# Kernel tuning notes

Hardware: AMD Instinct MI355X
Metric: run time of the kernel (lower is better)

Reference implementation:

```python
import jax, jax.numpy as jnp
import numpy as np

B, D, H = 1024, 64, 512


def setup_inputs() -> dict:
    key = jax.random.key(0)
    ks = jax.random.split(key, 6)
    sc = lambda fan_in: 1.0 / np.sqrt(fan_in)
    return {
        "x_t": jax.random.normal(ks[0], (B, D), jnp.float32),
        "t": jax.random.uniform(ks[1], (B, 1), dtype=jnp.float32),
        "beta": jax.random.uniform(ks[2], (B, 1), dtype=jnp.float32),
        "W1": jax.random.normal(ks[3], (D + 1, H), jnp.float32) * sc(D + 1),
        "b1": jnp.zeros((H,), jnp.float32),
        "W2": jax.random.normal(ks[4], (H, H), jnp.float32) * sc(H),
        "b2": jnp.zeros((H,), jnp.float32),
        "W3": jax.random.normal(ks[5], (H, D), jnp.float32) * sc(H),
        "b3": jnp.zeros((D,), jnp.float32),
    }


def _score(W1, b1, W2, b2, W3, b3, x, t):
    # x: [D], t: [1] -> s: [D]; small tanh MLP score network s(x, t)
    h = jnp.tanh(jnp.concatenate([x, t]) @ W1 + b1)
    h = jnp.tanh(h @ W2 + b2)
    return h @ W3 + b3


def reference(x_t, t, beta, W1, b1, W2, b2, W3, b3):
    def per_sample(x, tt):
        s_x = lambda xx: _score(W1, b1, W2, b2, W3, b3, xx, tt)
        s_t_fn = lambda ttt: _score(W1, b1, W2, b2, W3, b3, x, ttt)

        # s_t = grad(sum(s), t): sum over output dims of ds/dt (forward-mode JVP)
        _, s_dot = jax.jvp(s_t_fn, (tt,), (jnp.ones_like(tt),))
        s_t = jnp.sum(s_dot)  # scalar per sample

        # phi(x) = div_x s + |s|^2 + <s, x>; loss term = grad_x phi (2nd order through div)
        def phi(xx):
            jac = jax.jacfwd(s_x)(xx)          # [D, D]
            div = jnp.trace(jac)
            s = s_x(xx)
            return div + jnp.sum(s * s) + jnp.dot(s, xx)

        g = jax.grad(phi)(x)  # [D]
        return s_t, g

    s_t, g = jax.vmap(per_sample)(x_t, t)  # s_t: [B], g: [B, D]
    # loss = mean_D |s_t - 0.5 * beta * grad|, shape [B, 1]
    return jnp.mean(jnp.abs(s_t[:, None] - 0.5 * beta * g), axis=1, keepdims=True)
```

## Files before the change

### kernel.cpp

```cpp
#include <hip/hip_runtime.h>
#include <math.h>


#define Bsz 1024
#define Dd  64
#define Hh  512

__global__ __launch_bounds__(256) void kpre(const float* __restrict__ W1,
                                            const float* __restrict__ W3,
                                            const float* __restrict__ W2,
                                            float* __restrict__ C,
                                            float* __restrict__ W3T,
                                            float* __restrict__ W1xT,
                                            float* __restrict__ w3sum,
                                            float* __restrict__ s_t) {
  const int b = blockIdx.x;
  const int tid = threadIdx.x;
  if (b < 64) {
    __shared__ float W1s[64][68];
    __shared__ float W3s[64][68];
    const int bj = (b & 7) * 64, bl = (b >> 3) * 64;
    for (int q = 0; q < 16; q++) {
      int idx = tid + q * 256;
      int i = idx >> 6, j = idx & 63;
      W1s[i][j] = W1[i * Hh + bj + j];
    }
    for (int q = 0; q < 16; q++) {
      int idx = tid + q * 256;
      int l = idx >> 6, i = idx & 63;
      W3s[i][l] = W3[(bl + l) * Dd + i];
    }
    __syncthreads();
    const int tj = (tid >> 4) << 2, tl = (tid & 15) << 2;
    float acc[4][4] = {};
#pragma unroll 8
    for (int i = 0; i < 64; i++) {
      float4 a = *(const float4*)&W1s[i][tj];
      float4 bb = *(const float4*)&W3s[i][tl];
      float ar[4] = {a.x, a.y, a.z, a.w};
      float br[4] = {bb.x, bb.y, bb.z, bb.w};
#pragma unroll
      for (int r = 0; r < 4; r++)
#pragma unroll
        for (int c = 0; c < 4; c++) acc[r][c] += ar[r] * br[c];
    }
#pragma unroll
    for (int r = 0; r < 4; r++) {
      int j = bj + tj + r;
      float4 cv;
#pragma unroll
      for (int c = 0; c < 4; c++)
        ((float*)&cv)[c] = W2[j * Hh + bl + tl + c] * acc[r][c];
      *(float4*)&C[j * Hh + bl + tl] = cv;
    }
  } else {
    int gid = (b - 64) * 256 + tid;
#pragma unroll
    for (int q = 0; q < 8; q++) {
      int e = gid + q * 4096;
      int l = e >> 6, k = e & 63;
      W3T[k * Hh + l] = W3[e];
    }
#pragma unroll
    for (int q = 0; q < 8; q++) {
      int e = gid + q * 4096;
      int i = e >> 9, j = e & 511;
      W1xT[j * Dd + i] = W1[e];
    }
    if (gid < Hh) {
      float sacc = 0.f;
      for (int k = 0; k < 64; k++) sacc += W3[gid * Dd + k];
      w3sum[gid] = sacc;
    }
    if (gid < Bsz) s_t[gid] = 0.f;
  }
}

__global__ __launch_bounds__(256) void k1_h1(const float* __restrict__ X,
                                             const float* __restrict__ tt,
                                             const float* __restrict__ W1,
                                             const float* __restrict__ b1,
                                             float* __restrict__ h1,
                                             float* __restrict__ a1,
                                             float* __restrict__ dh1t) {
  __shared__ float As[64][68];
  __shared__ float Bs[64][68];
  const int i0 = blockIdx.x * 64, n0 = blockIdx.y * 64;
  const int tid = threadIdx.x;
  for (int q = 0; q < 16; q++) {
    int idx = tid + q * 256;
    int i = idx >> 6, k = idx & 63;
    As[k][i] = X[(i0 + i) * Dd + k];
  }
  for (int q = 0; q < 16; q++) {
    int idx = tid + q * 256;
    int k = idx >> 6, n = idx & 63;
    Bs[k][n] = W1[k * Hh + n0 + n];
  }
  __syncthreads();
  const int ti = (tid >> 4) << 2, tn = (tid & 15) << 2;
  float acc[4][4] = {};
#pragma unroll 8
  for (int k = 0; k < 64; k++) {
    float4 a = *(const float4*)&As[k][ti];
    float4 b = *(const float4*)&Bs[k][tn];
    float ar[4] = {a.x, a.y, a.z, a.w};
    float br[4] = {b.x, b.y, b.z, b.w};
#pragma unroll
    for (int r = 0; r < 4; r++)
#pragma unroll
      for (int c = 0; c < 4; c++) acc[r][c] += ar[r] * br[c];
  }
  const int nb = n0 + tn;
  float4 wtv = *(const float4*)&W1[Dd * Hh + nb];
  float4 b1v = *(const float4*)&b1[nb];
#pragma unroll
  for (int r = 0; r < 4; r++) {
    int i = i0 + ti + r;
    float tv = tt[i];
    float4 hv, av, dv;
#pragma unroll
    for (int c = 0; c < 4; c++) {
      float wt = ((float*)&wtv)[c];
      float z = acc[r][c] + tv * wt + ((float*)&b1v)[c];
      float h = tanhf(z);
      float a = 1.f - h * h;
      ((float*)&hv)[c] = h;
      ((float*)&av)[c] = a;
      ((float*)&dv)[c] = a * wt;
    }
    *(float4*)&h1[i * Hh + nb] = hv;
    *(float4*)&a1[i * Hh + nb] = av;
    *(float4*)&dh1t[i * Hh + nb] = dv;
  }
}

__global__ __launch_bounds__(256) void k2_h2(const float* __restrict__ h1,
                                             const float* __restrict__ dh1t,
                                             const float* __restrict__ W2,
                                             const float* __restrict__ b2,
                                             const float* __restrict__ w3s,
                                             float* __restrict__ h2,
                                             float* __restrict__ a2,
                                             float* __restrict__ s_t) {
  __shared__ float A1s[32][36], A2s[32][36], Bs[32][68];
  const int i0 = blockIdx.x * 32, n0 = blockIdx.y * 64;
  const int tid = threadIdx.x;
  const int ti = (tid >> 4) << 1, tn = (tid & 15) << 2;
  const int ai = tid >> 5, ak = tid & 31;
  const int bk = tid >> 6, bn = tid & 63;
  float ra1[4], ra2[4], rb[8];
#pragma unroll
  for (int q = 0; q < 4; q++) {
    ra1[q] = h1[(i0 + ai + q * 8) * Hh + ak];
    ra2[q] = dh1t[(i0 + ai + q * 8) * Hh + ak];
  }
#pragma unroll
  for (int q = 0; q < 8; q++) rb[q] = W2[(bk + q * 4) * Hh + n0 + bn];
  float acc1[2][4] = {}, acc2[2][4] = {};
  for (int c = 0; c < 16; c++) {
    __syncthreads();
#pragma unroll
    for (int q = 0; q < 4; q++) {
      A1s[ak][ai + q * 8] = ra1[q];
      A2s[ak][ai + q * 8] = ra2[q];
    }
#pragma unroll
    for (int q = 0; q < 8; q++) Bs[bk + q * 4][bn] = rb[q];
    __syncthreads();
    if (c < 15) {
      int k0 = (c + 1) * 32;
#pragma unroll
      for (int q = 0; q < 4; q++) {
        ra1[q] = h1[(i0 + ai + q * 8) * Hh + k0 + ak];
        ra2[q] = dh1t[(i0 + ai + q * 8) * Hh + k0 + ak];
      }
#pragma unroll
      for (int q = 0; q < 8; q++) rb[q] = W2[(k0 + bk + q * 4) * Hh + n0 + bn];
    }
#pragma unroll 8
    for (int k = 0; k < 32; k++) {
      float2 a1v = *(const float2*)&A1s[k][ti];
      float2 a2v = *(const float2*)&A2s[k][ti];
      float4 bv = *(const float4*)&Bs[k][tn];
      float ar1[2] = {a1v.x, a1v.y}, ar2[2] = {a2v.x, a2v.y};
      float br[4] = {bv.x, bv.y, bv.z, bv.w};
#pragma unroll
      for (int r = 0; r < 2; r++)
#pragma unroll
        for (int cc = 0; cc < 4; cc++) {
          acc1[r][cc] += ar1[r] * br[cc];
          acc2[r][cc] += ar2[r] * br[cc];
        }
    }
  }
  const int nb = n0 + tn;
  float4 b2v = *(const float4*)&b2[nb];
  float4 w3v = *(const float4*)&w3s[nb];
#pragma unroll
  for (int r = 0; r < 2; r++) {
    int i = i0 + ti + r;
    float4 hv, av;
    float part = 0.f;
#pragma unroll
    for (int cc = 0; cc < 4; cc++) {
      float z = acc1[r][cc] + ((float*)&b2v)[cc];
      float h = tanhf(z);
      float a = 1.f - h * h;
      ((float*)&hv)[cc] = h;
      ((float*)&av)[cc] = a;
      part += a * acc2[r][cc] * ((float*)&w3v)[cc];
    }
    *(float4*)&h2[i * Hh + nb] = hv;
    *(float4*)&a2[i * Hh + nb] = av;
#pragma unroll
    for (int off = 1; off < 16; off <<= 1) part += __shfl_xor(part, off, 64);
    if ((tid & 15) == 0) atomicAdd(&s_t[i], part);
  }
}

__global__ __launch_bounds__(256) void k34_s_r3(const float* __restrict__ h2,
                                                const float* __restrict__ W3,
                                                const float* __restrict__ W3T,
                                                const float* __restrict__ b3,
                                                const float* __restrict__ X,
                                                float* __restrict__ s,
                                                float* __restrict__ r3) {
  int i = (blockIdx.x * 256 + threadIdx.x) >> 6;
  int lam = threadIdx.x & 63;
  float sacc = b3[lam];
#pragma unroll
  for (int c = 0; c < 8; c++) {
    float hv = h2[i * Hh + c * 64 + lam];
#pragma unroll 8
    for (int k = 0; k < 64; k++) {
      float h = __shfl(hv, k, 64);
      sacc += h * W3[(c * 64 + k) * Dd + lam];
    }
  }
  s[i * Dd + lam] = sacc;
  float yv = 2.f * sacc + X[i * Dd + lam];
#pragma unroll
  for (int c = 0; c < 8; c++) {
    float acc = 0.f;
#pragma unroll 8
    for (int k = 0; k < 64; k++) {
      float yk = __shfl(yv, k, 64);
      acc += yk * W3T[k * Hh + c * 64 + lam];
    }
    r3[i * Hh + c * 64 + lam] = acc;
  }
}

__global__ __launch_bounds__(256) void k4b_ut2(const float* __restrict__ a1,
                                               const float* __restrict__ a2,
                                               const float* __restrict__ h2,
                                               const float* __restrict__ r3,
                                               const float* __restrict__ C,
                                               float* __restrict__ u,
                                               float* __restrict__ t2) {
  __shared__ float A1s[32][36], A2s[32][36], Bus[32][68], Bvs[32][68];
  const int i0 = blockIdx.x * 32, n0 = blockIdx.y * 64;
  const int tid = threadIdx.x;
  const int ti = (tid >> 4) << 1, tn = (tid & 15) << 2;
  const int ai = tid >> 5, ak = tid & 31;
  const int bk = tid >> 6, bn = tid & 63;
  const int un = tid >> 5, uk = tid & 31;
  float ra1[4], ra2[4], rbu[8], rbv[8];
#pragma unroll
  for (int q = 0; q < 4; q++) {
    ra2[q] = a2[(i0 + ai + q * 8) * Hh + ak];
    ra1[q] = a1[(i0 + ai + q * 8) * Hh + ak];
  }
#pragma unroll
  for (int q = 0; q < 8; q++) {
    rbu[q] = C[(n0 + un + q * 8) * Hh + uk];
    rbv[q] = C[(bk + q * 4) * Hh + n0 + bn];
  }
  float accU[2][4] = {}, accV[2][4] = {};
  for (int c = 0; c < 16; c++) {
    __syncthreads();
#pragma unroll
    for (int q = 0; q < 4; q++) {
      A1s[ak][ai + q * 8] = ra1[q];
      A2s[ak][ai + q * 8] = ra2[q];
    }
#pragma unroll
    for (int q = 0; q < 8; q++) {
      Bus[uk][un + q * 8] = rbu[q];
      Bvs[bk + q * 4][bn] = rbv[q];
    }
    __syncthreads();
    if (c < 15) {
      int k0 = (c + 1) * 32;
#pragma unroll
      for (int q = 0; q < 4; q++) {
        ra2[q] = a2[(i0 + ai + q * 8) * Hh + k0 + ak];
        ra1[q] = a1[(i0 + ai + q * 8) * Hh + k0 + ak];
      }
#pragma unroll
      for (int q = 0; q < 8; q++) {
        rbu[q] = C[(n0 + un + q * 8) * Hh + k0 + uk];
        rbv[q] = C[(k0 + bk + q * 4) * Hh + n0 + bn];
      }
    }
#pragma unroll 8
    for (int k = 0; k < 32; k++) {
      float2 a2v = *(const float2*)&A2s[k][ti];
      float2 a1v = *(const float2*)&A1s[k][ti];
      float4 bu = *(const float4*)&Bus[k][tn];
      float4 bv = *(const float4*)&Bvs[k][tn];
      float ar2[2] = {a2v.x, a2v.y}, ar1[2] = {a1v.x, a1v.y};
      float bur[4] = {bu.x, bu.y, bu.z, bu.w};
      float bvr[4] = {bv.x, bv.y, bv.z, bv.w};
#pragma unroll
      for (int r = 0; r < 2; r++)
#pragma unroll
        for (int cc = 0; cc < 4; cc++) {
          accU[r][cc] += ar2[r] * bur[cc];
          accV[r][cc] += ar1[r] * bvr[cc];
        }
    }
  }
  const int nb = n0 + tn;
#pragma unroll
  for (int r = 0; r < 2; r++) {
    int i = i0 + ti + r;
    float4 a2f = *(const float4*)&a2[i * Hh + nb];
    float4 h2f = *(const float4*)&h2[i * Hh + nb];
    float4 r3f = *(const float4*)&r3[i * Hh + nb];
    float4 uv, t2v;
#pragma unroll
    for (int cc = 0; cc < 4; cc++) {
      ((float*)&uv)[cc] = accU[r][cc];
      ((float*)&t2v)[cc] = ((float*)&a2f)[cc] *
          (((float*)&r3f)[cc] - 2.f * ((float*)&h2f)[cc] * accV[r][cc]);
    }
    *(float4*)&u[i * Hh + nb] = uv;
    *(float4*)&t2[i * Hh + nb] = t2v;
  }
}

__global__ __launch_bounds__(256) void k5_p(const float* __restrict__ t2,
                                            const float* __restrict__ W2,
                                            const float* __restrict__ a1,
                                            const float* __restrict__ h1,
                                            const float* __restrict__ u,
                                            float* __restrict__ p) {
  __shared__ float As[32][36], Bts[32][68];
  const int i0 = blockIdx.x * 32, n0 = blockIdx.y * 64;
  const int tid = threadIdx.x;
  const int ti = (tid >> 4) << 1, tn = (tid & 15) << 2;
  const int ai = tid >> 5, ak = tid & 31;
  const int un = tid >> 5, uk = tid & 31;
  float ra[4], rb[8];
#pragma unroll
  for (int q = 0; q < 4; q++) ra[q] = t2[(i0 + ai + q * 8) * Hh + ak];
#pragma unroll
  for (int q = 0; q < 8; q++) rb[q] = W2[(n0 + un + q * 8) * Hh + uk];
  float acc[2][4] = {};
  for (int c = 0; c < 16; c++) {
    __syncthreads();
#pragma unroll
    for (int q = 0; q < 4; q++) As[ak][ai + q * 8] = ra[q];
#pragma unroll
    for (int q = 0; q < 8; q++) Bts[uk][un + q * 8] = rb[q];
    __syncthreads();
    if (c < 15) {
      int k0 = (c + 1) * 32;
#pragma unroll
      for (int q = 0; q < 4; q++) ra[q] = t2[(i0 + ai + q * 8) * Hh + k0 + ak];
#pragma unroll
      for (int q = 0; q < 8; q++) rb[q] = W2[(n0 + un + q * 8) * Hh + k0 + uk];
    }
#pragma unroll 8
    for (int k = 0; k < 32; k++) {
      float2 av = *(const float2*)&As[k][ti];
      float4 bv = *(const float4*)&Bts[k][tn];
      float ar[2] = {av.x, av.y};
      float br[4] = {bv.x, bv.y, bv.z, bv.w};
#pragma unroll
      for (int r = 0; r < 2; r++)
#pragma unroll
        for (int cc = 0; cc < 4; cc++) acc[r][cc] += ar[r] * br[cc];
    }
  }
  const int nb = n0 + tn;
#pragma unroll
  for (int r = 0; r < 2; r++) {
    int i = i0 + ti + r;
    float4 a1f = *(const float4*)&a1[i * Hh + nb];
    float4 h1f = *(const float4*)&h1[i * Hh + nb];
    float4 uf  = *(const float4*)&u[i * Hh + nb];
    float4 pv;
#pragma unroll
    for (int cc = 0; cc < 4; cc++)
      ((float*)&pv)[cc] = ((float*)&a1f)[cc] *
          (acc[r][cc] - 2.f * ((float*)&h1f)[cc] * ((float*)&uf)[cc]);
    *(float4*)&p[i * Hh + nb] = pv;
  }
}

__global__ __launch_bounds__(256) void k6_loss(const float* __restrict__ p,
                                               const float* __restrict__ W1xT,
                                               const float* __restrict__ s,
                                               const float* __restrict__ s_t,
                                               const float* __restrict__ beta,
                                               float* __restrict__ out) {
  int i = (blockIdx.x * 256 + threadIdx.x) >> 6;
  int lam = threadIdx.x & 63;
  float g = s[i * Dd + lam];
#pragma unroll
  for (int c = 0; c < 8; c++) {
    float pv = p[i * Hh + c * 64 + lam];
#pragma unroll 8
    for (int jj = 0; jj < 64; jj++) {
      float pj = __shfl(pv, jj, 64);
      g += pj * W1xT[(c * 64 + jj) * Dd + lam];
    }
  }
  float e = fabsf(s_t[i] - 0.5f * beta[i] * g);
#pragma unroll
  for (int off = 32; off; off >>= 1) e += __shfl_down(e, off, 64);
  if (lam == 0) out[i] = e * (1.f / 64.f);
}

extern "C" void kernel_launch(void* const* d_in, const int* in_sizes, int n_in,
                              void* d_out, int out_size, void* d_ws, size_t ws_size,
                              hipStream_t stream) {
  const float* X    = (const float*)d_in[0];
  const float* tt   = (const float*)d_in[1];
  const float* beta = (const float*)d_in[2];
  const float* W1   = (const float*)d_in[3];
  const float* b1   = (const float*)d_in[4];
  const float* W2   = (const float*)d_in[5];
  const float* b2   = (const float*)d_in[6];
  const float* W3   = (const float*)d_in[7];
  const float* b3   = (const float*)d_in[8];
  float* out = (float*)d_out;

  float* ws   = (float*)d_ws;
  float* C    = ws;
  float* W3T  = C + 262144;
  float* W1xT = W3T + 32768;
  float* w3s  = W1xT + 32768;
  float* h1   = w3s + 512;
  float* a1   = h1 + 524288;
  float* dh1t = a1 + 524288;
  float* h2   = dh1t + 524288;
  float* a2v  = h2 + 524288;
  float* r3   = a2v + 524288;
  float* uu   = r3 + 524288;
  float* t2   = uu + 524288;
  float* pp   = t2 + 524288;
  float* ss   = pp + 524288;
  float* st   = ss + 65536;

  kpre<<<80, 256, 0, stream>>>(W1, W3, W2, C, W3T, W1xT, w3s, st);
  k1_h1<<<dim3(16, 8), 256, 0, stream>>>(X, tt, W1, b1, h1, a1, dh1t);
  k2_h2<<<dim3(32, 8), 256, 0, stream>>>(h1, dh1t, W2, b2, w3s, h2, a2v, st);
  k34_s_r3<<<256, 256, 0, stream>>>(h2, W3, W3T, b3, X, ss, r3);
  k4b_ut2<<<dim3(32, 8), 256, 0, stream>>>(a1, a2v, h2, r3, C, uu, t2);
  k5_p<<<dim3(32, 8), 256, 0, stream>>>(t2, W2, a1, h1, uu, pp);
  k6_loss<<<256, 256, 0, stream>>>(pp, W1xT, ss, st, beta, out);
}
```

Baseline: 239.8 us.

## Fuse per-sample forward/backward pipeline into one kernel with shared-memory activations

Replaces six launches (h1, h2, s/r3, u/t2, p, loss) with a single kernel in which each 512-thread block handles 4 samples and keeps all intermediate activations in shared memory. The goal is to drop the global-memory round trips for the many [B,H] intermediates, the launch overheads, and the atomics used for s_t. In exchange, every block streams the full W1, W2, W3 and C weight matrices from global or L2 for only 4 samples, so weight reuse per block is much lower and the work becomes matrix-vector-like. Some C reads are column-strided (C[k*Hh+n0]) while others are row reads that are not coalesced across threads.

```diff
diff --git a/kernel.cpp b/kernel.cpp
--- a/kernel.cpp
+++ b/kernel.cpp
@@ -10,10 +10,7 @@
                                             const float* __restrict__ W3,
                                             const float* __restrict__ W2,
                                             float* __restrict__ C,
-                                            float* __restrict__ W3T,
-                                            float* __restrict__ W1xT,
-                                            float* __restrict__ w3sum,
-                                            float* __restrict__ s_t) {
+                                            float* __restrict__ w3sum) {
   const int b = blockIdx.x;
   const int tid = threadIdx.x;
   if (b < 64) {
@@ -54,375 +51,223 @@
       *(float4*)&C[j * Hh + bl + tl] = cv;
     }
   } else {
-    int gid = (b - 64) * 256 + tid;
-#pragma unroll
-    for (int q = 0; q < 8; q++) {
-      int e = gid + q * 4096;
-      int l = e >> 6, k = e & 63;
-      W3T[k * Hh + l] = W3[e];
-    }
-#pragma unroll
-    for (int q = 0; q < 8; q++) {
-      int e = gid + q * 4096;
-      int i = e >> 9, j = e & 511;
-      W1xT[j * Dd + i] = W1[e];
-    }
-    if (gid < Hh) {
+#pragma unroll
+    for (int r = 0; r < 2; r++) {
+      int n = tid + r * 256;
       float sacc = 0.f;
-      for (int k = 0; k < 64; k++) sacc += W3[gid * Dd + k];
-      w3sum[gid] = sacc;
-    }
-    if (gid < Bsz) s_t[gid] = 0.f;
+#pragma unroll 4
+      for (int k4 = 0; k4 < 16; k4++) {
+        float4 w = *(const float4*)&W3[n * Dd + k4 * 4];
+        sacc += w.x; sacc += w.y; sacc += w.z; sacc += w.w;
+      }
+      w3sum[n] = sacc;
+    }
   }
 }
 
-__global__ __launch_bounds__(256) void k1_h1(const float* __restrict__ X,
-                                             const float* __restrict__ tt,
-                                             const float* __restrict__ W1,
-                                             const float* __restrict__ b1,
-                                             float* __restrict__ h1,
-                                             float* __restrict__ a1,
-                                             float* __restrict__ dh1t) {
-  __shared__ float As[64][68];
-  __shared__ float Bs[64][68];
-  const int i0 = blockIdx.x * 64, n0 = blockIdx.y * 64;
+__global__ __launch_bounds__(512) void kfused(const float* __restrict__ X,
+                                              const float* __restrict__ tt,
+                                              const float* __restrict__ beta,
+                                              const float* __restrict__ W1,
+                                              const float* __restrict__ b1,
+                                              const float* __restrict__ W2,
+                                              const float* __restrict__ b2,
+                                              const float* __restrict__ W3,
+                                              const float* __restrict__ b3,
+                                              const float* __restrict__ C,
+                                              const float* __restrict__ w3sum,
+                                              float* __restrict__ out) {
+  __shared__ float xs[Dd * 4], ys[Dd * 4];
+  __shared__ float h1s[Hh * 4], a1s[Hh * 4], q1s[Hh * 4];
+  __shared__ float h2s[Hh * 4], a2s[Hh * 4], t2s[Hh * 4], ps[Hh * 4];
+  __shared__ float sts[4], tb[4], bb4[4], red[32];
+  __shared__ float ph[512];
+
   const int tid = threadIdx.x;
-  for (int q = 0; q < 16; q++) {
-    int idx = tid + q * 256;
-    int i = idx >> 6, k = idx & 63;
-    As[k][i] = X[(i0 + i) * Dd + k];
-  }
-  for (int q = 0; q < 16; q++) {
-    int idx = tid + q * 256;
-    int k = idx >> 6, n = idx & 63;
-    Bs[k][n] = W1[k * Hh + n0 + n];
-  }
-  __syncthreads();
-  const int ti = (tid >> 4) << 2, tn = (tid & 15) << 2;
-  float acc[4][4] = {};
-#pragma unroll 8
-  for (int k = 0; k < 64; k++) {
-    float4 a = *(const float4*)&As[k][ti];
-    float4 b = *(const float4*)&Bs[k][tn];
-    float ar[4] = {a.x, a.y, a.z, a.w};
-    float br[4] = {b.x, b.y, b.z, b.w};
-#pragma unroll
-    for (int r = 0; r < 4; r++)
-#pragma unroll
-      for (int c = 0; c < 4; c++) acc[r][c] += ar[r] * br[c];
-  }
-  const int nb = n0 + tn;
-  float4 wtv = *(const float4*)&W1[Dd * Hh + nb];
-  float4 b1v = *(const float4*)&b1[nb];
-#pragma unroll
-  for (int r = 0; r < 4; r++) {
-    int i = i0 + ti + r;
-    float tv = tt[i];
-    float4 hv, av, dv;
-#pragma unroll
-    for (int c = 0; c < 4; c++) {
-      float wt = ((float*)&wtv)[c];
-      float z = acc[r][c] + tv * wt + ((float*)&b1v)[c];
+  const int s0 = blockIdx.x * 4;
+  const int n0 = tid;
+  const int dd = tid & 63;
+  const int half = (tid >> 6) & 1;
+  const int ss = tid >> 7;
+
+  if (tid < 256) {
+    int sA = tid >> 6, dA = tid & 63;
+    xs[dA * 4 + sA] = X[(s0 + sA) * Dd + dA];
+  }
+  if (tid < 4) tb[tid] = tt[s0 + tid];
+  else if (tid < 8) bb4[tid - 4] = beta[s0 + tid - 4];
+  __syncthreads();
+
+  {
+    float acc[4] = {};
+#pragma unroll 8
+    for (int k = 0; k < Dd; k++) {
+      float w = W1[k * Hh + n0];
+      float4 xv = *(const float4*)&xs[k * 4];
+#pragma unroll
+      for (int s = 0; s < 4; s++) acc[s] += w * ((float*)&xv)[s];
+    }
+    float wt = W1[Dd * Hh + n0];
+    float bc = b1[n0];
+    float4 hv, av, qv;
+#pragma unroll
+    for (int s = 0; s < 4; s++) {
+      float z = acc[s] + tb[s] * wt + bc;
       float h = tanhf(z);
       float a = 1.f - h * h;
-      ((float*)&hv)[c] = h;
-      ((float*)&av)[c] = a;
-      ((float*)&dv)[c] = a * wt;
-    }
-    *(float4*)&h1[i * Hh + nb] = hv;
-    *(float4*)&a1[i * Hh + nb] = av;
-    *(float4*)&dh1t[i * Hh + nb] = dv;
-  }
-}
-
-__global__ __launch_bounds__(256) void k2_h2(const float* __restrict__ h1,
-                                             const float* __restrict__ dh1t,
-                                             const float* __restrict__ W2,
-                                             const float* __restrict__ b2,
-                                             const float* __restrict__ w3s,
-                                             float* __restrict__ h2,
-                                             float* __restrict__ a2,
-                                             float* __restrict__ s_t) {
-  __shared__ float A1s[32][36], A2s[32][36], Bs[32][68];
-  const int i0 = blockIdx.x * 32, n0 = blockIdx.y * 64;
-  const int tid = threadIdx.x;
-  const int ti = (tid >> 4) << 1, tn = (tid & 15) << 2;
-  const int ai = tid >> 5, ak = tid & 31;
-  const int bk = tid >> 6, bn = tid & 63;
-  float ra1[4], ra2[4], rb[8];
-#pragma unroll
-  for (int q = 0; q < 4; q++) {
-    ra1[q] = h1[(i0 + ai + q * 8) * Hh + ak];
-    ra2[q] = dh1t[(i0 + ai + q * 8) * Hh + ak];
-  }
-#pragma unroll
-  for (int q = 0; q < 8; q++) rb[q] = W2[(bk + q * 4) * Hh + n0 + bn];
-  float acc1[2][4] = {}, acc2[2][4] = {};
-  for (int c = 0; c < 16; c++) {
-    __syncthreads();
-#pragma unroll
-    for (int q = 0; q < 4; q++) {
-      A1s[ak][ai + q * 8] = ra1[q];
-      A2s[ak][ai + q * 8] = ra2[q];
-    }
-#pragma unroll
-    for (int q = 0; q < 8; q++) Bs[bk + q * 4][bn] = rb[q];
-    __syncthreads();
-    if (c < 15) {
-      int k0 = (c + 1) * 32;
-#pragma unroll
-      for (int q = 0; q < 4; q++) {
-        ra1[q] = h1[(i0 + ai + q * 8) * Hh + k0 + ak];
-        ra2[q] = dh1t[(i0 + ai + q * 8) * Hh + k0 + ak];
-      }
-#pragma unroll
-      for (int q = 0; q < 8; q++) rb[q] = W2[(k0 + bk + q * 4) * Hh + n0 + bn];
-    }
-#pragma unroll 8
-    for (int k = 0; k < 32; k++) {
-      float2 a1v = *(const float2*)&A1s[k][ti];
-      float2 a2v = *(const float2*)&A2s[k][ti];
-      float4 bv = *(const float4*)&Bs[k][tn];
-      float ar1[2] = {a1v.x, a1v.y}, ar2[2] = {a2v.x, a2v.y};
-      float br[4] = {bv.x, bv.y, bv.z, bv.w};
-#pragma unroll
-      for (int r = 0; r < 2; r++)
-#pragma unroll
-        for (int cc = 0; cc < 4; cc++) {
-          acc1[r][cc] += ar1[r] * br[cc];
-          acc2[r][cc] += ar2[r] * br[cc];
-        }
-    }
-  }
-  const int nb = n0 + tn;
-  float4 b2v = *(const float4*)&b2[nb];
-  float4 w3v = *(const float4*)&w3s[nb];
-#pragma unroll
-  for (int r = 0; r < 2; r++) {
-    int i = i0 + ti + r;
+      ((float*)&hv)[s] = h;
+      ((float*)&av)[s] = a;
+      ((float*)&qv)[s] = a * wt;
+    }
+    *(float4*)&h1s[n0 * 4] = hv;
+    *(float4*)&a1s[n0 * 4] = av;
+    *(float4*)&q1s[n0 * 4] = qv;
+  }
+  __syncthreads();
+
+  {
+    float acc1[4] = {}, acc2[4] = {};
+#pragma unroll 8
+    for (int k = 0; k < Hh; k++) {
+      float w = W2[k * Hh + n0];
+      float4 hv = *(const float4*)&h1s[k * 4];
+      float4 qv = *(const float4*)&q1s[k * 4];
+#pragma unroll
+      for (int s = 0; s < 4; s++) {
+        acc1[s] += w * ((float*)&hv)[s];
+        acc2[s] += w * ((float*)&qv)[s];
+      }
+    }
+    float bc = b2[n0], wc = w3sum[n0];
+    float stp[4];
     float4 hv, av;
-    float part = 0.f;
-#pragma unroll
-    for (int cc = 0; cc < 4; cc++) {
-      float z = acc1[r][cc] + ((float*)&b2v)[cc];
+#pragma unroll
+    for (int s = 0; s < 4; s++) {
+      float z = acc1[s] + bc;
       float h = tanhf(z);
       float a = 1.f - h * h;
-      ((float*)&hv)[cc] = h;
-      ((float*)&av)[cc] = a;
-      part += a * acc2[r][cc] * ((float*)&w3v)[cc];
-    }
-    *(float4*)&h2[i * Hh + nb] = hv;
-    *(float4*)&a2[i * Hh + nb] = av;
-#pragma unroll
-    for (int off = 1; off < 16; off <<= 1) part += __shfl_xor(part, off, 64);
-    if ((tid & 15) == 0) atomicAdd(&s_t[i], part);
-  }
-}
-
-__global__ __launch_bounds__(256) void k34_s_r3(const float* __restrict__ h2,
-                                                const float* __restrict__ W3,
-                                                const float* __restrict__ W3T,
-                                                const float* __restrict__ b3,
-                                                const float* __restrict__ X,
-                                                float* __restrict__ s,
-                                                float* __restrict__ r3) {
-  int i = (blockIdx.x * 256 + threadIdx.x) >> 6;
-  int lam = threadIdx.x & 63;
-  float sacc = b3[lam];
-#pragma unroll
-  for (int c = 0; c < 8; c++) {
-    float hv = h2[i * Hh + c * 64 + lam];
-#pragma unroll 8
-    for (int k = 0; k < 64; k++) {
-      float h = __shfl(hv, k, 64);
-      sacc += h * W3[(c * 64 + k) * Dd + lam];
-    }
-  }
-  s[i * Dd + lam] = sacc;
-  float yv = 2.f * sacc + X[i * Dd + lam];
-#pragma unroll
-  for (int c = 0; c < 8; c++) {
-    float acc = 0.f;
-#pragma unroll 8
-    for (int k = 0; k < 64; k++) {
-      float yk = __shfl(yv, k, 64);
-      acc += yk * W3T[k * Hh + c * 64 + lam];
-    }
-    r3[i * Hh + c * 64 + lam] = acc;
-  }
-}
-
-__global__ __launch_bounds__(256) void k4b_ut2(const float* __restrict__ a1,
-                                               const float* __restrict__ a2,
-                                               const float* __restrict__ h2,
-                                               const float* __restrict__ r3,
-                                               const float* __restrict__ C,
-                                               float* __restrict__ u,
-                                               float* __restrict__ t2) {
-  __shared__ float A1s[32][36], A2s[32][36], Bus[32][68], Bvs[32][68];
-  const int i0 = blockIdx.x * 32, n0 = blockIdx.y * 64;
-  const int tid = threadIdx.x;
-  const int ti = (tid >> 4) << 1, tn = (tid & 15) << 2;
-  const int ai = tid >> 5, ak = tid & 31;
-  const int bk = tid >> 6, bn = tid & 63;
-  const int un = tid >> 5, uk = tid & 31;
-  float ra1[4], ra2[4], rbu[8], rbv[8];
-#pragma unroll
-  for (int q = 0; q < 4; q++) {
-    ra2[q] = a2[(i0 + ai + q * 8) * Hh + ak];
-    ra1[q] = a1[(i0 + ai + q * 8) * Hh + ak];
-  }
-#pragma unroll
-  for (int q = 0; q < 8; q++) {
-    rbu[q] = C[(n0 + un + q * 8) * Hh + uk];
-    rbv[q] = C[(bk + q * 4) * Hh + n0 + bn];
-  }
-  float accU[2][4] = {}, accV[2][4] = {};
-  for (int c = 0; c < 16; c++) {
-    __syncthreads();
-#pragma unroll
-    for (int q = 0; q < 4; q++) {
-      A1s[ak][ai + q * 8] = ra1[q];
-      A2s[ak][ai + q * 8] = ra2[q];
-    }
-#pragma unroll
-    for (int q = 0; q < 8; q++) {
-      Bus[uk][un + q * 8] = rbu[q];
-      Bvs[bk + q * 4][bn] = rbv[q];
-    }
-    __syncthreads();
-    if (c < 15) {
-      int k0 = (c + 1) * 32;
-#pragma unroll
-      for (int q = 0; q < 4; q++) {
-        ra2[q] = a2[(i0 + ai + q * 8) * Hh + k0 + ak];
-        ra1[q] = a1[(i0 + ai + q * 8) * Hh + k0 + ak];
-      }
-#pragma unroll
-      for (int q = 0; q < 8; q++) {
-        rbu[q] = C[(n0 + un + q * 8) * Hh + k0 + uk];
-        rbv[q] = C[(k0 + bk + q * 4) * Hh + n0 + bn];
-      }
-    }
-#pragma unroll 8
-    for (int k = 0; k < 32; k++) {
-      float2 a2v = *(const float2*)&A2s[k][ti];
-      float2 a1v = *(const float2*)&A1s[k][ti];
-      float4 bu = *(const float4*)&Bus[k][tn];
-      float4 bv = *(const float4*)&Bvs[k][tn];
-      float ar2[2] = {a2v.x, a2v.y}, ar1[2] = {a1v.x, a1v.y};
-      float bur[4] = {bu.x, bu.y, bu.z, bu.w};
-      float bvr[4] = {bv.x, bv.y, bv.z, bv.w};
-#pragma unroll
-      for (int r = 0; r < 2; r++)
-#pragma unroll
-        for (int cc = 0; cc < 4; cc++) {
-          accU[r][cc] += ar2[r] * bur[cc];
-          accV[r][cc] += ar1[r] * bvr[cc];
+      ((float*)&hv)[s] = h;
+      ((float*)&av)[s] = a;
+      stp[s] = a * acc2[s] * wc;
+    }
+    *(float4*)&h2s[n0 * 4] = hv;
+    *(float4*)&a2s[n0 * 4] = av;
+#pragma unroll
+    for (int off = 1; off < 64; off <<= 1)
+#pragma unroll
+      for (int s = 0; s < 4; s++) stp[s] += __shfl_xor(stp[s], off, 64);
+    if (dd == 0)
+#pragma unroll
+      for (int s = 0; s < 4; s++) red[(tid >> 6) * 4 + s] = stp[s];
+  }
+  __syncthreads();
+  if (tid < 4) {
+    float t = 0.f;
+#pragma unroll
+    for (int w = 0; w < 8; w++) t += red[w * 4 + tid];
+    sts[tid] = t;
+  }
+
+  {
+    float sacc = half ? 0.f : b3[dd];
+    const int l0 = half * 256;
+#pragma unroll 8
+    for (int l = l0; l < l0 + 256; l++)
+      sacc += W3[l * Dd + dd] * h2s[l * 4 + ss];
+    ph[tid] = sacc;
+  }
+  __syncthreads();
+  float sval = 0.f;
+  if (half == 0) {
+    sval = ph[ss * 128 + dd] + ph[ss * 128 + 64 + dd];
+    ys[dd * 4 + ss] = 2.f * sval + xs[dd * 4 + ss];
+  }
+  __syncthreads();
+
+  float ua[4] = {};
+  {
+    float r3a[4] = {};
+#pragma unroll 4
+    for (int k4 = 0; k4 < 16; k4++) {
+      float4 w = *(const float4*)&W3[n0 * Dd + k4 * 4];
+#pragma unroll
+      for (int j = 0; j < 4; j++) {
+        float4 yv = *(const float4*)&ys[(k4 * 4 + j) * 4];
+#pragma unroll
+        for (int s = 0; s < 4; s++) r3a[s] += ((float*)&w)[j] * ((float*)&yv)[s];
+      }
+    }
+    float va[4] = {};
+#pragma unroll 2
+    for (int k4 = 0; k4 < 128; k4++) {
+      float4 cu = *(const float4*)&C[n0 * Hh + k4 * 4];
+#pragma unroll
+      for (int j = 0; j < 4; j++) {
+        int k = k4 * 4 + j;
+        float cv = C[k * Hh + n0];
+        float4 a1v = *(const float4*)&a1s[k * 4];
+        float4 a2v = *(const float4*)&a2s[k * 4];
+#pragma unroll
+        for (int s = 0; s < 4; s++) {
+          va[s] += cv * ((float*)&a1v)[s];
+          ua[s] += ((float*)&cu)[j] * ((float*)&a2v)[s];
         }
-    }
-  }
-  const int nb = n0 + tn;
-#pragma unroll
-  for (int r = 0; r < 2; r++) {
-    int i = i0 + ti + r;
-    float4 a2f = *(const float4*)&a2[i * Hh + nb];
-    float4 h2f = *(const float4*)&h2[i * Hh + nb];
-    float4 r3f = *(const float4*)&r3[i * Hh + nb];
-    float4 uv, t2v;
-#pragma unroll
-    for (int cc = 0; cc < 4; cc++) {
-      ((float*)&uv)[cc] = accU[r][cc];
-      ((float*)&t2v)[cc] = ((float*)&a2f)[cc] *
-          (((float*)&r3f)[cc] - 2.f * ((float*)&h2f)[cc] * accV[r][cc]);
-    }
-    *(float4*)&u[i * Hh + nb] = uv;
-    *(float4*)&t2[i * Hh + nb] = t2v;
-  }
-}
-
-__global__ __launch_bounds__(256) void k5_p(const float* __restrict__ t2,
-                                            const float* __restrict__ W2,
-                                            const float* __restrict__ a1,
-                                            const float* __restrict__ h1,
-                                            const float* __restrict__ u,
-                                            float* __restrict__ p) {
-  __shared__ float As[32][36], Bts[32][68];
-  const int i0 = blockIdx.x * 32, n0 = blockIdx.y * 64;
-  const int tid = threadIdx.x;
-  const int ti = (tid >> 4) << 1, tn = (tid & 15) << 2;
-  const int ai = tid >> 5, ak = tid & 31;
-  const int un = tid >> 5, uk = tid & 31;
-  float ra[4], rb[8];
-#pragma unroll
-  for (int q = 0; q < 4; q++) ra[q] = t2[(i0 + ai + q * 8) * Hh + ak];
-#pragma unroll
-  for (int q = 0; q < 8; q++) rb[q] = W2[(n0 + un + q * 8) * Hh + uk];
-  float acc[2][4] = {};
-  for (int c = 0; c < 16; c++) {
-    __syncthreads();
-#pragma unroll
-    for (int q = 0; q < 4; q++) As[ak][ai + q * 8] = ra[q];
-#pragma unroll
-    for (int q = 0; q < 8; q++) Bts[uk][un + q * 8] = rb[q];
-    __syncthreads();
-    if (c < 15) {
-      int k0 = (c + 1) * 32;
-#pragma unroll
-      for (int q = 0; q < 4; q++) ra[q] = t2[(i0 + ai + q * 8) * Hh + k0 + ak];
-#pragma unroll
-      for (int q = 0; q < 8; q++) rb[q] = W2[(n0 + un + q * 8) * Hh + k0 + uk];
-    }
-#pragma unroll 8
-    for (int k = 0; k < 32; k++) {
-      float2 av = *(const float2*)&As[k][ti];
-      float4 bv = *(const float4*)&Bts[k][tn];
-      float ar[2] = {av.x, av.y};
-      float br[4] = {bv.x, bv.y, bv.z, bv.w};
-#pragma unroll
-      for (int r = 0; r < 2; r++)
-#pragma unroll
-        for (int cc = 0; cc < 4; cc++) acc[r][cc] += ar[r] * br[cc];
-    }
-  }
-  const int nb = n0 + tn;
-#pragma unroll
-  for (int r = 0; r < 2; r++) {
-    int i = i0 + ti + r;
-    float4 a1f = *(const float4*)&a1[i * Hh + nb];
-    float4 h1f = *(const float4*)&h1[i * Hh + nb];
-    float4 uf  = *(const float4*)&u[i * Hh + nb];
+      }
+    }
+    float4 a2r = *(const float4*)&a2s[n0 * 4];
+    float4 h2r = *(const float4*)&h2s[n0 * 4];
+    float4 t2v;
+#pragma unroll
+    for (int s = 0; s < 4; s++)
+      ((float*)&t2v)[s] = ((float*)&a2r)[s] *
+          (r3a[s] - 2.f * ((float*)&h2r)[s] * va[s]);
+    *(float4*)&t2s[n0 * 4] = t2v;
+  }
+  __syncthreads();
+
+  {
+    float pa[4] = {};
+#pragma unroll 2
+    for (int k4 = 0; k4 < 128; k4++) {
+      float4 w = *(const float4*)&W2[n0 * Hh + k4 * 4];
+#pragma unroll
+      for (int j = 0; j < 4; j++) {
+        float4 t2v = *(const float4*)&t2s[(k4 * 4 + j) * 4];
+#pragma unroll
+        for (int s = 0; s < 4; s++) pa[s] += ((float*)&w)[j] * ((float*)&t2v)[s];
+      }
+    }
+    float4 a1r = *(const float4*)&a1s[n0 * 4];
+    float4 h1r = *(const float4*)&h1s[n0 * 4];
     float4 pv;
 #pragma unroll
-    for (int cc = 0; cc < 4; cc++)
-      ((float*)&pv)[cc] = ((float*)&a1f)[cc] *
-          (acc[r][cc] - 2.f * ((float*)&h1f)[cc] * ((float*)&uf)[cc]);
-    *(float4*)&p[i * Hh + nb] = pv;
-  }
-}
-
-__global__ __launch_bounds__(256) void k6_loss(const float* __restrict__ p,
-                                               const float* __restrict__ W1xT,
-                                               const float* __restrict__ s,
-                                               const float* __restrict__ s_t,
-                                               const float* __restrict__ beta,
-                                               float* __restrict__ out) {
-  int i = (blockIdx.x * 256 + threadIdx.x) >> 6;
-  int lam = threadIdx.x & 63;
-  float g = s[i * Dd + lam];
-#pragma unroll
-  for (int c = 0; c < 8; c++) {
-    float pv = p[i * Hh + c * 64 + lam];
-#pragma unroll 8
-    for (int jj = 0; jj < 64; jj++) {
-      float pj = __shfl(pv, jj, 64);
-      g += pj * W1xT[(c * 64 + jj) * Dd + lam];
-    }
-  }
-  float e = fabsf(s_t[i] - 0.5f * beta[i] * g);
-#pragma unroll
-  for (int off = 32; off; off >>= 1) e += __shfl_down(e, off, 64);
-  if (lam == 0) out[i] = e * (1.f / 64.f);
+    for (int s = 0; s < 4; s++)
+      ((float*)&pv)[s] = ((float*)&a1r)[s] *
+          (pa[s] - 2.f * ((float*)&h1r)[s] * ua[s]);
+    *(float4*)&ps[n0 * 4] = pv;
+  }
+  __syncthreads();
+
+  {
+    float g = (half == 0) ? sval : 0.f;
+    const int j0 = half * 256;
+#pragma unroll 4
+    for (int j4 = 0; j4 < 64; j4++) {
+      float4 w = *(const float4*)&W1[dd * Hh + j0 + j4 * 4];
+#pragma unroll
+      for (int j = 0; j < 4; j++)
+        g += ((float*)&w)[j] * ps[(j0 + j4 * 4 + j) * 4 + ss];
+    }
+    ph[tid] = g;
+  }
+  __syncthreads();
+  if (half == 0) {
+    float g = ph[ss * 128 + dd] + ph[ss * 128 + 64 + dd];
+    float e = fabsf(sts[ss] - 0.5f * bb4[ss] * g);
+#pragma unroll
+    for (int off = 32; off; off >>= 1) e += __shfl_down(e, off, 64);
+    if (dd == 0) out[s0 + ss] = e * (1.f / 64.f);
+  }
 }
 
 extern "C" void kernel_launch(void* const* d_in, const int* in_sizes, int n_in,
@@ -439,28 +284,10 @@
   const float* b3   = (const float*)d_in[8];
   float* out = (float*)d_out;
 
-  float* ws   = (float*)d_ws;
-  float* C    = ws;
-  float* W3T  = C + 262144;
-  float* W1xT = W3T + 32768;
-  float* w3s  = W1xT + 32768;
-  float* h1   = w3s + 512;
-  float* a1   = h1 + 524288;
-  float* dh1t = a1 + 524288;
-  float* h2   = dh1t + 524288;
-  float* a2v  = h2 + 524288;
-  float* r3   = a2v + 524288;
-  float* uu   = r3 + 524288;
-  float* t2   = uu + 524288;
-  float* pp   = t2 + 524288;
-  float* ss   = pp + 524288;
-  float* st   = ss + 65536;
-
-  kpre<<<80, 256, 0, stream>>>(W1, W3, W2, C, W3T, W1xT, w3s, st);
-  k1_h1<<<dim3(16, 8), 256, 0, stream>>>(X, tt, W1, b1, h1, a1, dh1t);
-  k2_h2<<<dim3(32, 8), 256, 0, stream>>>(h1, dh1t, W2, b2, w3s, h2, a2v, st);
-  k34_s_r3<<<256, 256, 0, stream>>>(h2, W3, W3T, b3, X, ss, r3);
-  k4b_ut2<<<dim3(32, 8), 256, 0, stream>>>(a1, a2v, h2, r3, C, uu, t2);
-  k5_p<<<dim3(32, 8), 256, 0, stream>>>(t2, W2, a1, h1, uu, pp);
-  k6_loss<<<256, 256, 0, stream>>>(pp, W1xT, ss, st, beta, out);
+  float* ws  = (float*)d_ws;
+  float* C   = ws;
+  float* w3s = C + 262144;
+
+  kpre<<<65, 256, 0, stream>>>(W1, W3, W2, C, w3s);
+  kfused<<<256, 512, 0, stream>>>(X, tt, beta, W1, b1, W2, b2, W3, b3, C, w3s, out);
 }
```

Result: faster. 199.1 us (-17.0%).
